# Optimization experiments

Measured on AMD Instinct MI355X. Metric: run time of the kernel, lower is better.

## Reference

```python
import jax, jax.numpy as jnp
import numpy as np

ALPHA = 0.1        # axis_aligned_projection threshold
NEG_INF = -1e30    # large negative used for masking (softmax-equivalent to -inf)


def axis_aligned_projection(x, alpha=ALPHA):
    x_abs = jnp.abs(x)
    max_vals = jnp.max(x_abs, axis=-1, keepdims=True)
    axis_weights = jnp.where(x_abs >= alpha * max_vals, x_abs, 0.0)
    return axis_weights * jnp.sign(x)


def setup_inputs() -> dict:
    key = jax.random.key(0)
    kq, kk, kv = jax.random.split(key, 3)
    B, L, H, E = 4, 2048, 8, 64
    S, D = L, E
    queries = jax.random.normal(kq, (B, L, H, E), dtype=jnp.float32)
    keys = jax.random.normal(kk, (B, S, H, E), dtype=jnp.float32)
    values = jax.random.normal(kv, (B, S, H, D), dtype=jnp.float32)
    # TriangularCausalMask: True strictly above the diagonal -> masked out
    causal = jnp.triu(jnp.ones((L, S), dtype=jnp.bool_), k=1)
    attn_mask = jnp.broadcast_to(causal[None, None], (B, 1, L, S))
    return {"queries": queries, "keys": keys, "values": values, "attn_mask": attn_mask}


def reference(queries, keys, values, attn_mask):
    B, L, H, E = queries.shape
    scale = 1.0 / jnp.sqrt(jnp.float32(E))
    q = axis_aligned_projection(queries)
    k = axis_aligned_projection(keys)
    # [B,H,L,S] dense scores (the module materializes the full matrix)
    scores = jnp.einsum('blhe,bshe->bhls', q, k)
    scores = jnp.where(attn_mask, NEG_INF, scores)
    A = jax.nn.softmax(scale * scores, axis=-1)  # dropout is identity in eval mode
    V = jnp.einsum('bhls,bshd->blhd', A, values)
    return V
```

## Files before the change

### kernel.cpp

```cpp
#include <hip/hip_runtime.h>
#include <hip/hip_bf16.h>
#include <stdint.h>

#define B_ 4
#define L_ 2048
#define H_ 8
#define E_ 64
#define ALPHA 0.1f
#define LOG2E 1.44269504088896f
#define QSCALE (0.125f * LOG2E)


typedef float f32x4 __attribute__((ext_vector_type(4)));
typedef short bf16x8 __attribute__((ext_vector_type(8)));
typedef short bf16x4 __attribute__((ext_vector_type(4)));
typedef uint32_t u32;
typedef unsigned short u16;
typedef u32 u32x2 __attribute__((ext_vector_type(2)));

__device__ __forceinline__ u16 f2bf(float f) {
    u32 x = __builtin_bit_cast(u32, f);
    u32 r = x + 0x7fffu + ((x >> 16) & 1u);
    return (u16)(r >> 16);
}

__device__ __forceinline__ u32 pk2bf(float a, float b) {
    u32 ua = __builtin_bit_cast(u32, a) + 0x8000u;
    u32 ub = __builtin_bit_cast(u32, b) + 0x8000u;
    return (ua >> 16) | (ub & 0xffff0000u);
}

__device__ __forceinline__ f32x4 mfma16x16x16bf16(bf16x4 a, bf16x4 b, f32x4 c) {
#if __has_builtin(__builtin_amdgcn_mfma_f32_16x16x16bf16_1k)
    return __builtin_amdgcn_mfma_f32_16x16x16bf16_1k(a, b, c, 0, 0, 0);
#elif __has_builtin(__builtin_amdgcn_mfma_f32_16x16x16_bf16)
    return __builtin_amdgcn_mfma_f32_16x16x16_bf16(a, b, c, 0, 0, 0);
#else
    f32x4 d;
    asm volatile("v_mfma_f32_16x16x16_bf16 %0, %1, %2, %3"
                 : "=v"(d) : "v"(a), "v"(b), "v"(c));
    return d;
#endif
}

__device__ __forceinline__ void dma16(const u16* g, u16* l) {
    __builtin_amdgcn_global_load_lds(
        (const __attribute__((address_space(1))) void*)g,
        (__attribute__((address_space(3))) void*)l, 16, 0, 0);
}

__global__ __launch_bounds__(256) void prep_kernel(const float* __restrict__ qin,
                                                   const float* __restrict__ kin,
                                                   const float* __restrict__ vin,
                                                   u16* __restrict__ qp,
                                                   u16* __restrict__ kp,
                                                   u16* __restrict__ vt) {
    __shared__ u16 tile[64][66];
    if (blockIdx.x < 4096) {
        const int RG = (B_ * L_ * H_) / 8;
        int wave = threadIdx.x >> 6, lane = threadIdx.x & 63;
        int g = blockIdx.x * 4 + wave;
        const float* src;
        u16* dst;
        int gr;
        float sc;
        bool isq;
        if (g < RG) { src = qin; dst = qp; gr = g; sc = QSCALE; isq = true; }
        else        { src = kin; dst = kp; gr = g - RG; sc = 1.0f; isq = false; }

        int rig = lane >> 3;
        int j = lane & 7;
        int c = j * 4;
        int row = gr * 8 + rig;

        const float* rp = src + (size_t)row * 64;
        float4 v0 = *(const float4*)(rp + c);
        float4 v1 = *(const float4*)(rp + c + 32);
        float f[8] = {v0.x, v0.y, v0.z, v0.w, v1.x, v1.y, v1.z, v1.w};

        float mx = 0.f;
#pragma unroll
        for (int i = 0; i < 8; ++i) mx = fmaxf(mx, fabsf(f[i]));
#pragma unroll
        for (int m = 1; m < 8; m <<= 1) mx = fmaxf(mx, __shfl_xor(mx, m));
        float thr = ALPHA * mx;

        u16 o[8];
#pragma unroll
        for (int i = 0; i < 8; ++i)
            o[i] = (fabsf(f[i]) >= thr) ? f2bf(f[i] * sc) : (u16)0;

        int b = row >> 14;
        int l = (row >> 3) & (L_ - 1);
        int h = row & 7;
        int e0, e1;
        if (isq) {
            e0 = c;
            e1 = c + 32;
        } else {
            int l7 = l & 7;
            e0 = (((j >> 1) ^ l7) << 3) + ((j & 1) << 2);
            e1 = ((((j >> 1) + 4) ^ l7) << 3) + ((j & 1) << 2);
        }
        u16* orow = dst + ((size_t)(b * H_ + h) * L_ + l) * 64;
        uint2 p0 = {(u32)o[0] | ((u32)o[1] << 16), (u32)o[2] | ((u32)o[3] << 16)};
        uint2 p1 = {(u32)o[4] | ((u32)o[5] << 16), (u32)o[6] | ((u32)o[7] << 16)};
        *(uint2*)(orow + e0) = p0;
        *(uint2*)(orow + e1) = p1;
    } else {
        int bx = blockIdx.x - 4096;
        int bh = bx >> 5, sblk = bx & 31;
        int b = bh >> 3, h = bh & 7;
        int t = threadIdx.x;
        int s0 = sblk * 64;

#pragma unroll
        for (int p = 0; p < 2; ++p) {
            int sl = p * 32 + (t >> 3);
            int c = (t & 7) * 4;
            const float* rp = vin + (((size_t)(b * L_ + s0 + sl)) * H_ + h) * 64;
            float4 a = *(const float4*)(rp + c);
            float4 bb = *(const float4*)(rp + c + 32);
            u32* d0 = (u32*)&tile[sl][c];
            d0[0] = (u32)f2bf(a.x) | ((u32)f2bf(a.y) << 16);
            d0[1] = (u32)f2bf(a.z) | ((u32)f2bf(a.w) << 16);
            u32* d1 = (u32*)&tile[sl][c + 32];
            d1[0] = (u32)f2bf(bb.x) | ((u32)f2bf(bb.y) << 16);
            d1[1] = (u32)f2bf(bb.z) | ((u32)f2bf(bb.w) << 16);
        }
        __syncthreads();
#pragma unroll
        for (int p = 0; p < 2; ++p) {
            int d = p * 32 + (t >> 3);
            int c16 = t & 7;
            int sc2 = c16 * 8;
            u16 o[8];
#pragma unroll
            for (int i = 0; i < 8; ++i) o[i] = tile[sc2 + i][d];
            u32 w0 = (u32)o[0] | ((u32)o[1] << 16);
            u32 w1 = (u32)o[2] | ((u32)o[3] << 16);
            u32 w2 = (u32)o[4] | ((u32)o[5] << 16);
            u32 w3 = (u32)o[6] | ((u32)o[7] << 16);
            uint4 val;
            if (d & 1) { val.x = w2; val.y = w3; val.z = w0; val.w = w1; }
            else       { val.x = w0; val.y = w1; val.z = w2; val.w = w3; }
            int pc = c16 ^ ((d >> 1) & 7);
            *(uint4*)(vt + ((size_t)(bh * 32 + sblk) * 64 + d) * 64 + pc * 8) = val;
        }
    }
}

__global__ __launch_bounds__(256, 4) void flash_kernel(const u16* __restrict__ Qp,
                                                       const u16* __restrict__ Kp,
                                                       const u16* __restrict__ Vt,
                                                       float* __restrict__ out) {
    __shared__ u16 kbuf[2][64 * 64];
    __shared__ u16 vbuf[2][64 * 64];
    int t = threadIdx.x;
    int wave = t >> 6, lane = t & 63;
    int bh = blockIdx.x & 31;
    int r5 = blockIdx.x >> 5;
    int g = r5 & 7, kr = r5 >> 3;
    int qq = (kr == 0) ? (31 - g) : (kr == 1) ? (16 + g) : (kr == 2) ? (15 - g) : g;
    int lo = lane & 15, quad = lane >> 4;
    int lo7 = lo & 7;
    int q0 = qq * 64 + wave * 16;
    int b = bh >> 3, h = bh & 7;

    int kc0 = (quad ^ lo7) << 3;
    int kc1 = ((quad + 4) ^ lo7) << 3;

    u32x2 onespk = {0x3F803F80u, 0x3F803F80u};
    bf16x4 vONES = __builtin_bit_cast(bf16x4, onespk);

    const u16* kg0 = Kp + (size_t)bh * L_ * 64 + wave * 512 + lane * 8;
    const u16* vg0 = Vt + (size_t)bh * 32 * 64 * 64 + wave * 512 + lane * 8;

    auto stage = [&](int kt, int buf) {
        const u16* kg = kg0 + (size_t)kt * 4096;
        const u16* vg = vg0 + (size_t)kt * 4096;
        u16* kl = kbuf[buf] + wave * 512;
        u16* vl = vbuf[buf] + wave * 512;
        dma16(kg, kl);
        dma16(kg + 2048, kl + 2048);
        dma16(vg, vl);
        dma16(vg + 2048, vl + 2048);
    };

    const u16* qbase = Qp + ((size_t)bh * L_ + q0 + lo) * 64 + quad * 8;
    bf16x8 aQ0 = *(const bf16x8*)(qbase);
    bf16x8 aQ1 = *(const bf16x8*)(qbase + 32);
    asm volatile("" :: "v"(aQ0), "v"(aQ1));

    f32x4 o[4];
#pragma unroll
    for (int ni = 0; ni < 4; ++ni) o[ni] = (f32x4){0.f, 0.f, 0.f, 0.f};
    f32x4 oL = (f32x4){0.f, 0.f, 0.f, 0.f};

    auto tile_proc = [&](const u16* ks, const u16* vs) {
        bf16x8 k0[4], k1[4];
#pragma unroll
        for (int sub = 0; sub < 4; ++sub) {
            const u16* krow = ks + ((sub * 16 + lo) << 6);
            k0[sub] = *(const bf16x8*)(krow + kc0);
            k1[sub] = *(const bf16x8*)(krow + kc1);
        }
        bf16x4 vf[4][4];
#pragma unroll
        for (int sub = 0; sub < 4; ++sub) {
            int vsw = ((sub * 4 + quad) ^ lo) << 2;
#pragma unroll
            for (int ni = 0; ni < 4; ++ni)
                vf[sub][ni] = *(const bf16x4*)(vs + ((ni * 16 + lo) << 6) + vsw);
        }
        __builtin_amdgcn_s_setprio(1);
        f32x4 S[4];
#pragma unroll
        for (int sub = 0; sub < 4; ++sub) {
            f32x4 acc = {0.f, 0.f, 0.f, 0.f};
            acc = __builtin_amdgcn_mfma_f32_16x16x32_bf16(k0[sub], aQ0, acc, 0, 0, 0);
            S[sub] = __builtin_amdgcn_mfma_f32_16x16x32_bf16(k1[sub], aQ1, acc, 0, 0, 0);
        }
        bf16x4 aP[4];
#pragma unroll
        for (int sub = 0; sub < 4; ++sub) {
            float P0 = __builtin_amdgcn_exp2f(S[sub][0]);
            float P1 = __builtin_amdgcn_exp2f(S[sub][1]);
            float P2 = __builtin_amdgcn_exp2f(S[sub][2]);
            float P3 = __builtin_amdgcn_exp2f(S[sub][3]);
            u32x2 pk = {pk2bf(P0, P1), pk2bf(P2, P3)};
            aP[sub] = __builtin_bit_cast(bf16x4, pk);
        }
#pragma unroll
        for (int sub = 0; sub < 4; ++sub) {
#pragma unroll
            for (int ni = 0; ni < 4; ++ni)
                o[ni] = mfma16x16x16bf16(aP[sub], vf[sub][ni], o[ni]);
            oL = mfma16x16x16bf16(aP[sub], vONES, oL);
        }
        __builtin_amdgcn_s_setprio(0);
    };

    auto frag_proc = [&](const u16* ks, const u16* vs, int sub, bool diag) {
        const u16* krow = ks + ((sub * 16 + lo) << 6);
        bf16x8 k0 = *(const bf16x8*)(krow + kc0);
        bf16x8 k1 = *(const bf16x8*)(krow + kc1);
        f32x4 S = {0.f, 0.f, 0.f, 0.f};
        S = __builtin_amdgcn_mfma_f32_16x16x32_bf16(k0, aQ0, S, 0, 0, 0);
        S = __builtin_amdgcn_mfma_f32_16x16x32_bf16(k1, aQ1, S, 0, 0, 0);

        int vsw = ((sub * 4 + quad) ^ lo) << 2;
        bf16x4 vf[4];
#pragma unroll
        for (int ni = 0; ni < 4; ++ni)
            vf[ni] = *(const bf16x4*)(vs + ((ni * 16 + lo) << 6) + vsw);

        float P[4];
#pragma unroll
        for (int r = 0; r < 4; ++r) {
            float e = __builtin_amdgcn_exp2f(S[r]);
            P[r] = (diag && (quad * 4 + r > lo)) ? 0.f : e;
        }
        u32x2 pk = {pk2bf(P[0], P[1]), pk2bf(P[2], P[3])};
        bf16x4 aP = __builtin_bit_cast(bf16x4, pk);
#pragma unroll
        for (int ni = 0; ni < 4; ++ni)
            o[ni] = mfma16x16x16bf16(aP, vf[ni], o[ni]);
        oL = mfma16x16x16bf16(aP, vONES, oL);
    };

    stage(0, 0);
    __syncthreads();

    for (int kt = 0; kt < qq; ++kt) {
        int cur = kt & 1;
        stage(kt + 1, cur ^ 1);
        tile_proc(kbuf[cur], vbuf[cur]);
        __syncthreads();
    }

    {
        int cur = qq & 1;
        const u16* ks = kbuf[cur];
        const u16* vs = vbuf[cur];
        __builtin_amdgcn_s_setprio(1);
        for (int sub = 0; sub < wave; ++sub) frag_proc(ks, vs, sub, false);
        frag_proc(ks, vs, wave, true);
        __builtin_amdgcn_s_setprio(0);
    }

#pragma unroll
    for (int r = 0; r < 4; ++r) {
        float inv = 1.0f / oL[r];
        int q = q0 + quad * 4 + r;
        float* ob = out + (((size_t)(b * L_ + q)) * H_ + h) * 64 + lo;
        ob[0]  = o[0][r] * inv;
        ob[16] = o[1][r] * inv;
        ob[32] = o[2][r] * inv;
        ob[48] = o[3][r] * inv;
    }
}

extern "C" void kernel_launch(void* const* d_in, const int* in_sizes, int n_in,
                              void* d_out, int out_size, void* d_ws, size_t ws_size,
                              hipStream_t stream) {
    const float* q = (const float*)d_in[0];
    const float* k = (const float*)d_in[1];
    const float* v = (const float*)d_in[2];
    float* out = (float*)d_out;

    const size_t QSZ = (size_t)B_ * H_ * L_ * 64;
    u16* qp = (u16*)d_ws;
    u16* kp = qp + QSZ;
    u16* vt = kp + QSZ;

    prep_kernel<<<5120, 256, 0, stream>>>(q, k, v, qp, kp, vt);
    flash_kernel<<<1024, 256, 0, stream>>>(qp, kp, vt, out);
}
```

Measured before the change: 163.4 us.

## Split causal KV range across two blocks and add combine kernel

Each query tile's causal key range is split into two halves processed by separate blocks, doubling the grid and shortening the longest per-block chain. Unnormalized partial outputs and row sums go to workspace, and a new combine kernel adds them and normalizes. This relies on the kernel not using a running max, so partials add directly. It trades extra global memory traffic and a third kernel launch for better load balance and more parallelism.

```diff
diff --git a/kernel.cpp b/kernel.cpp
--- a/kernel.cpp
+++ b/kernel.cpp
@@ -153,19 +153,24 @@
 __global__ __launch_bounds__(256, 4) void flash_kernel(const u16* __restrict__ Qp,
                                                        const u16* __restrict__ Kp,
                                                        const u16* __restrict__ Vt,
-                                                       float* __restrict__ out) {
+                                                       float* __restrict__ pO,
+                                                       float* __restrict__ pL) {
     __shared__ u16 kbuf[2][64 * 64];
     __shared__ u16 vbuf[2][64 * 64];
     int t = threadIdx.x;
     int wave = t >> 6, lane = t & 63;
-    int bh = blockIdx.x & 31;
-    int r5 = blockIdx.x >> 5;
-    int g = r5 & 7, kr = r5 >> 3;
-    int qq = (kr == 0) ? (31 - g) : (kr == 1) ? (16 + g) : (kr == 2) ? (15 - g) : g;
+    int i = blockIdx.x;
+    int half = i & 1;
+    int tk = i >> 1;
+    int bh = tk & 31;
+    int qq = 31 - (tk >> 5);
     int lo = lane & 15, quad = lane >> 4;
     int lo7 = lo & 7;
     int q0 = qq * 64 + wave * 16;
-    int b = bh >> 3, h = bh & 7;
+
+    int h0 = (qq + 2) >> 1;
+    int s0 = half ? h0 : 0;
+    int s1 = half ? (qq + 1) : h0;
 
     int kc0 = (quad ^ lo7) << 3;
     int kc1 = ((quad + 4) ^ lo7) << 3;
@@ -269,35 +274,65 @@
         oL = mfma16x16x16bf16(aP, vONES, oL);
     };
 
-    stage(0, 0);
-    __syncthreads();
-
-    for (int kt = 0; kt < qq; ++kt) {
-        int cur = kt & 1;
-        stage(kt + 1, cur ^ 1);
-        tile_proc(kbuf[cur], vbuf[cur]);
+    if (s1 > s0) {
+        stage(s0, 0);
         __syncthreads();
+        int cur = 0;
+        for (int kt = s0; kt < s1 - 1; ++kt) {
+            stage(kt + 1, cur ^ 1);
+            tile_proc(kbuf[cur], vbuf[cur]);
+            __syncthreads();
+            cur ^= 1;
+        }
+        if (s1 - 1 == qq) {
+            const u16* ks = kbuf[cur];
+            const u16* vs = vbuf[cur];
+            __builtin_amdgcn_s_setprio(1);
+            for (int sub = 0; sub < wave; ++sub) frag_proc(ks, vs, sub, false);
+            frag_proc(ks, vs, wave, true);
+            __builtin_amdgcn_s_setprio(0);
+        } else {
+            tile_proc(kbuf[cur], vbuf[cur]);
+        }
     }
 
-    {
-        int cur = qq & 1;
-        const u16* ks = kbuf[cur];
-        const u16* vs = vbuf[cur];
-        __builtin_amdgcn_s_setprio(1);
-        for (int sub = 0; sub < wave; ++sub) frag_proc(ks, vs, sub, false);
-        frag_proc(ks, vs, wave, true);
-        __builtin_amdgcn_s_setprio(0);
+    int slot = ((qq * 32 + bh) << 1) + half;
+    float* pout = pO + (size_t)slot * 4096;
+    float* plp = pL + slot * 64;
+#pragma unroll
+    for (int r = 0; r < 4; ++r) {
+        int rr = wave * 16 + quad * 4 + r;
+        float* ob = pout + rr * 64 + lo;
+        ob[0]  = o[0][r];
+        ob[16] = o[1][r];
+        ob[32] = o[2][r];
+        ob[48] = o[3][r];
+        if (lo == 0) plp[rr] = oL[r];
     }
-
-#pragma unroll
-    for (int r = 0; r < 4; ++r) {
-        float inv = 1.0f / oL[r];
-        int q = q0 + quad * 4 + r;
-        float* ob = out + (((size_t)(b * L_ + q)) * H_ + h) * 64 + lo;
-        ob[0]  = o[0][r] * inv;
-        ob[16] = o[1][r] * inv;
-        ob[32] = o[2][r] * inv;
-        ob[48] = o[3][r] * inv;
+}
+
+__global__ __launch_bounds__(256) void combine_kernel(const float* __restrict__ pO,
+                                                      const float* __restrict__ pL,
+                                                      float* __restrict__ out) {
+    int c = blockIdx.x;
+    int qq = c >> 5, bh = c & 31;
+    int b = bh >> 3, h = bh & 7;
+    int t = threadIdx.x;
+    int rr = t >> 2;
+    int cq = (t & 3) * 16;
+    int slot0 = ((qq * 32 + bh) << 1);
+    const float* pa = pO + (size_t)slot0 * 4096 + rr * 64 + cq;
+    const float* pb = pa + 4096;
+    float l = pL[slot0 * 64 + rr] + pL[(slot0 + 1) * 64 + rr];
+    float inv = 1.0f / l;
+    int q = qq * 64 + rr;
+    float* ob = out + (((size_t)(b * L_ + q)) * H_ + h) * 64 + cq;
+#pragma unroll
+    for (int j = 0; j < 4; ++j) {
+        f32x4 va = *(const f32x4*)(pa + j * 4);
+        f32x4 vb = *(const f32x4*)(pb + j * 4);
+        f32x4 vr = (va + vb) * inv;
+        *(f32x4*)(ob + j * 4) = vr;
     }
 }
 
@@ -313,7 +348,10 @@
     u16* qp = (u16*)d_ws;
     u16* kp = qp + QSZ;
     u16* vt = kp + QSZ;
+    float* pO = (float*)(vt + QSZ);
+    float* pL = pO + (size_t)2048 * 4096;
 
     prep_kernel<<<5120, 256, 0, stream>>>(q, k, v, qp, kp, vt);
-    flash_kernel<<<1024, 256, 0, stream>>>(qp, kp, vt, out);
-}
+    flash_kernel<<<2048, 256, 0, stream>>>(qp, kp, vt, pO, pL);
+    combine_kernel<<<1024, 256, 0, stream>>>(pO, pL, out);
+}
```

Measured after the change: 167.2 us. +2.3%, slower.
